# Optimization experiments

Measured on AMD Instinct MI355X. Metric: run time of the kernel, lower is better.

The kernel has to match this reference:

```python
import jax, jax.numpy as jnp
import numpy as np

DELTA = 0.5  # fuzziness factor (module default)

def setup_inputs() -> dict:
    key = jax.random.key(0)
    kq, kk, kv = jax.random.split(key, 3)
    B, L, H, E = 2, 2048, 16, 64
    queries = jax.random.normal(kq, (B, L, H, E), jnp.float32)
    keys_ = jax.random.normal(kk, (B, L, H, E), jnp.float32)
    values = jax.random.normal(kv, (B, L, H, E), jnp.float32)
    # TriangularCausalMask: True above the diagonal -> masked out
    attn_mask = jnp.triu(jnp.ones((L, L), dtype=bool), k=1)[None, None]  # [1,1,L,L]
    return {"queries": queries, "keys": keys_, "values": values, "attn_mask": attn_mask}

def reference(queries, keys, values, attn_mask):
    # queries: [B,L,H,E], keys/values: [B,S,H,E], attn_mask: [1,1,L,S] bool (True = masked)
    E = queries.shape[-1]
    scale = 1.0 / np.sqrt(E)
    scores = jnp.einsum('blhe,bshe->bhls', queries, keys)  # [B,H,L,S]
    # fuzzy modification; note sigmoid(-inf)=0 so masking before or after is equivalent,
    # we mask after for grad safety
    fuzzy = scores + DELTA * jax.nn.sigmoid(scores)
    fuzzy = jnp.where(attn_mask, -jnp.inf, fuzzy)
    A = jax.nn.softmax(scale * fuzzy, axis=-1)  # dropout p=0 (eval mode)
    V = jnp.einsum('bhls,bshd->blhd', A, values)  # [B,L,H,D]
    return V
```

## Files before the change

kernel.cpp:

```cpp
#include <hip/hip_runtime.h>
#include <math.h>


typedef __bf16 bf16x8 __attribute__((ext_vector_type(8)));
typedef __bf16 bf16x4 __attribute__((ext_vector_type(4)));
typedef float  f32x4  __attribute__((ext_vector_type(4)));

constexpr int Lc = 2048, Hc = 16, Ec = 64;
constexpr int QBLK = 64, KVB = 64;
constexpr int NQT  = Lc / QBLK;
constexpr int ROWS = Hc * Ec;
constexpr float LOG2E = 1.4426950408889634f;
constexpr float C1 = 0.125f * LOG2E;
constexpr float C3 = 0.5f * 0.125f * LOG2E;

__global__ __launch_bounds__(256)
void conv_kv(const float* __restrict__ Kp, const float* __restrict__ Vp,
             __bf16* __restrict__ Kbf, __bf16* __restrict__ Vbf) {
    const int bid = blockIdx.x;
    const int tid = threadIdx.x;
    if (bid < 1024) {
        const int task = bid * 256 + tid;
        const int row = task >> 2, q4 = task & 3;
        const int h = row & 15, bl = row >> 4;
        const int b = bl >> 11, l = bl & 2047;
        const float4* src = reinterpret_cast<const float4*>(Kp + (size_t)row * 64 + q4 * 16);
        __bf16* dst = Kbf + ((size_t)((b * 16 + h) * 2048 + l)) * 64 + q4 * 16;
        float4 x0 = src[0], x1 = src[1], x2 = src[2], x3 = src[3];
        bf16x8 o0, o1;
        o0[0]=(__bf16)x0.x; o0[1]=(__bf16)x0.y; o0[2]=(__bf16)x0.z; o0[3]=(__bf16)x0.w;
        o0[4]=(__bf16)x1.x; o0[5]=(__bf16)x1.y; o0[6]=(__bf16)x1.z; o0[7]=(__bf16)x1.w;
        o1[0]=(__bf16)x2.x; o1[1]=(__bf16)x2.y; o1[2]=(__bf16)x2.z; o1[3]=(__bf16)x2.w;
        o1[4]=(__bf16)x3.x; o1[5]=(__bf16)x3.y; o1[6]=(__bf16)x3.z; o1[7]=(__bf16)x3.w;
        reinterpret_cast<bf16x8*>(dst)[0] = o0;
        reinterpret_cast<bf16x8*>(dst)[1] = o1;
    } else {
        __shared__ __bf16 tl[64 * 72];
        const int vb = bid - 1024;
        const int bh = vb >> 5, lt = vb & 31;
        const int b = bh >> 4, h = bh & 15;
        {
            const int l = tid >> 2, dc = tid & 3;
            const float4* src = reinterpret_cast<const float4*>(
                Vp + ((size_t)((b * 2048 + lt * 64 + l) * 16 + h)) * 64 + dc * 16);
            float4 v0 = src[0], v1 = src[1], v2 = src[2], v3 = src[3];
            float e[16] = {v0.x,v0.y,v0.z,v0.w, v1.x,v1.y,v1.z,v1.w,
                           v2.x,v2.y,v2.z,v2.w, v3.x,v3.y,v3.z,v3.w};
            #pragma unroll
            for (int i = 0; i < 16; ++i) tl[(dc * 16 + i) * 72 + l] = (__bf16)e[i];
        }
        __syncthreads();
        {
            const int d = tid >> 2, lc = tid & 3;
            bf16x8 a = *reinterpret_cast<const bf16x8*>(&tl[d * 72 + lc * 16]);
            bf16x8 c = *reinterpret_cast<const bf16x8*>(&tl[d * 72 + lc * 16 + 8]);
            __bf16* dst = Vbf + ((size_t)bh * 64 + d) * 2048 + lt * 64 + lc * 16;
            reinterpret_cast<bf16x8*>(dst)[0] = a;
            reinterpret_cast<bf16x8*>(dst)[1] = c;
        }
    }
}

__global__ __launch_bounds__(256, 4)
void fuzzy_attn_mfma(const float* __restrict__ Qp, const __bf16* __restrict__ Kbf,
                     const __bf16* __restrict__ Vbf, float* __restrict__ Op) {
    __shared__ __bf16 kt[2][KVB * Ec];
    __shared__ __bf16 vt[2][KVB * Ec];
    __shared__ __bf16 pt[4][1024];

    const int id  = blockIdx.x;
    const int xcd = id & 7;
    const int r_  = id >> 3;
    const int s4  = r_ & 3;
    const int qt  = (NQT - 1) - (r_ >> 2);
    const int bh  = s4 * 8 + xcd;
    const int b = bh >> 4, h = bh & 15;

    const int tid  = threadIdx.x;
    const int lane = tid & 63;
    const int w    = tid >> 6;
    const int q16  = lane & 15;
    const int g    = lane >> 4;
    const int qhalf  = w & 1;
    const int kvhalf = w >> 1;

    const __bf16* Kh = Kbf + (size_t)bh * (Lc * Ec);
    const __bf16* Vh = Vbf + (size_t)bh * (Ec * Lc);
    const float*  Qb = Qp + (size_t)b * Lc * ROWS + h * Ec;
    float*        Ob = Op + (size_t)b * Lc * ROWS + h * Ec;

    const int qrow0 = qt * QBLK + qhalf * 32 + q16;
    const int qrow1 = qrow0 + 16;

    const int srow0 = w * 8 + (lane >> 3);
    const int srow1 = srow0 + 32;
    const int sch0  = (lane & 7) ^ ((srow0 & 7) ^ (srow0 >> 3));
    const int sch1  = (lane & 7) ^ ((srow1 & 7) ^ (srow1 >> 3));
    const __bf16* kgA = Kh + srow0 * 64   + sch0 * 8;
    const __bf16* kgB = Kh + srow1 * 64   + sch1 * 8;
    const __bf16* vgA = Vh + srow0 * 2048 + sch0 * 8;
    const __bf16* vgB = Vh + srow1 * 2048 + sch1 * 8;

    bf16x8 qb[2][2];
    #pragma unroll
    for (int qs = 0; qs < 2; ++qs) {
        #pragma unroll
        for (int ks = 0; ks < 2; ++ks) {
            const float* qp = Qb + (size_t)(qs ? qrow1 : qrow0) * ROWS + g * 8 + 32 * ks;
            float4 x0 = reinterpret_cast<const float4*>(qp)[0];
            float4 x1 = reinterpret_cast<const float4*>(qp)[1];
            bf16x8 tq;
            tq[0]=(__bf16)x0.x; tq[1]=(__bf16)x0.y; tq[2]=(__bf16)x0.z; tq[3]=(__bf16)x0.w;
            tq[4]=(__bf16)x1.x; tq[5]=(__bf16)x1.y; tq[6]=(__bf16)x1.z; tq[7]=(__bf16)x1.w;
            qb[qs][ks] = tq;
        }
    }

    const int nst = qt + 1;

    #define STAGE(bufi, st_)                                                          \
        do {                                                                          \
            const __bf16* kga = kgA + (size_t)(st_) * (KVB * Ec);                     \
            const __bf16* kgb = kgB + (size_t)(st_) * (KVB * Ec);                     \
            const __bf16* vga = vgA + (st_) * KVB;                                    \
            const __bf16* vgb = vgB + (st_) * KVB;                                    \
            __builtin_amdgcn_global_load_lds(                                         \
                (const __attribute__((address_space(1))) void*)kga,                   \
                (__attribute__((address_space(3))) void*)&kt[bufi][w * 512], 16, 0, 0); \
            __builtin_amdgcn_global_load_lds(                                         \
                (const __attribute__((address_space(1))) void*)kgb,                   \
                (__attribute__((address_space(3))) void*)&kt[bufi][2048 + w * 512], 16, 0, 0); \
            __builtin_amdgcn_global_load_lds(                                         \
                (const __attribute__((address_space(1))) void*)vga,                   \
                (__attribute__((address_space(3))) void*)&vt[bufi][w * 512], 16, 0, 0); \
            __builtin_amdgcn_global_load_lds(                                         \
                (const __attribute__((address_space(1))) void*)vgb,                   \
                (__attribute__((address_space(3))) void*)&vt[bufi][2048 + w * 512], 16, 0, 0); \
        } while (0)

    STAGE(0, 0);

    float la0 = 0.f, la1 = 0.f;
    float lb0 = 0.f, lb1 = 0.f;
    f32x4 oacc[2][4];
    #pragma unroll
    for (int qs = 0; qs < 2; ++qs) {
        #pragma unroll
        for (int ds = 0; ds < 4; ++ds) { f32x4 z = {0.f,0.f,0.f,0.f}; oacc[qs][ds] = z; }
    }

    char* pw = reinterpret_cast<char*>(pt[w]);
    const int pswz = q16 & 3;

    for (int st = 0; st < nst; ++st) {
        const int buf = st & 1;
        __syncthreads();

        if (st + 1 < nst) STAGE(buf ^ 1, st + 1);

        const char* kbase = reinterpret_cast<const char*>(kt[buf]);
        const char* vbase = reinterpret_cast<const char*>(vt[buf]);

        f32x4 sacc[2][2];
        #pragma unroll
        for (int kv = 0; kv < 2; ++kv) {
            #pragma unroll
            for (int qs = 0; qs < 2; ++qs) { f32x4 z = {0.f,0.f,0.f,0.f}; sacc[kv][qs] = z; }
        }
        __builtin_amdgcn_s_setprio(1);
        #pragma unroll
        for (int kv = 0; kv < 2; ++kv) {
            const int kvr  = kvhalf * 32 + kv * 16 + q16;
            const int kkey = ((kvr & 7) ^ (kvr >> 3)) << 4;
            #pragma unroll
            for (int ks = 0; ks < 2; ++ks) {
                bf16x8 ka = *reinterpret_cast<const bf16x8*>(
                    kbase + kvr * 128 + (((g + 4 * ks) << 4) ^ kkey));
                sacc[kv][0] = __builtin_amdgcn_mfma_f32_16x16x32_bf16(ka, qb[0][ks], sacc[kv][0], 0, 0, 0);
                sacc[kv][1] = __builtin_amdgcn_mfma_f32_16x16x32_bf16(ka, qb[1][ks], sacc[kv][1], 0, 0, 0);
            }
        }
        __builtin_amdgcn_s_setprio(0);

        const bool diagm = (st == qt) && (kvhalf >= qhalf);
        #pragma unroll
        for (int kv = 0; kv < 2; ++kv) {
            #pragma unroll
            for (int qs = 0; qs < 2; ++qs) {
                const int qrow_s = qs ? qrow1 : qrow0;
                float p4[4];
                #pragma unroll
                for (int r = 0; r < 4; ++r) {
                    const float s  = sacc[kv][qs][r];
                    const float sg = __builtin_amdgcn_fmed3f(fmaf(s, 0.1875f, 0.5f), 0.f, 1.f);
                    float u = fmaf(sg, C3, s * C1);
                    if (diagm) {
                        const int kvg = st * KVB + kvhalf * 32 + kv * 16 + 4 * g + r;
                        if (kvg > qrow_s) u = -INFINITY;
                    }
                    p4[r] = __builtin_amdgcn_exp2f(u);
                }
                if (qs == 0) { la0 += p4[0] + p4[1]; la1 += p4[2] + p4[3]; }
                else         { lb0 += p4[0] + p4[1]; lb1 += p4[2] + p4[3]; }
                bf16x4 pk;
                pk[0]=(__bf16)p4[0]; pk[1]=(__bf16)p4[1]; pk[2]=(__bf16)p4[2]; pk[3]=(__bf16)p4[3];
                *reinterpret_cast<bf16x4*>(
                    pw + (qs * 16 + q16) * 64 +
                    (((2 * kv + (g >> 1)) ^ pswz) << 4) + (g & 1) * 8) = pk;
            }
        }

        bf16x8 pa0 = *reinterpret_cast<const bf16x8*>(
            pw + (0 * 16 + q16) * 64 + ((g ^ pswz) << 4));
        bf16x8 pa1 = *reinterpret_cast<const bf16x8*>(
            pw + (1 * 16 + q16) * 64 + ((g ^ pswz) << 4));
        __builtin_amdgcn_s_setprio(1);
        #pragma unroll
        for (int ds = 0; ds < 4; ++ds) {
            const int vrow = ds * 16 + q16;
            const int vkey = ((vrow & 7) ^ (vrow >> 3)) << 4;
            bf16x8 vb = *reinterpret_cast<const bf16x8*>(
                vbase + vrow * 128 + (((kvhalf * 4 + g) << 4) ^ vkey));
            oacc[0][ds] = __builtin_amdgcn_mfma_f32_16x16x32_bf16(pa0, vb, oacc[0][ds], 0, 0, 0);
            oacc[1][ds] = __builtin_amdgcn_mfma_f32_16x16x32_bf16(pa1, vb, oacc[1][ds], 0, 0, 0);
        }
        __builtin_amdgcn_s_setprio(0);
    }
    #undef STAGE

    float lr0 = la0 + la1;
    float lr1 = lb0 + lb1;
    lr0 += __shfl_xor(lr0, 16); lr0 += __shfl_xor(lr0, 32);
    lr1 += __shfl_xor(lr1, 16); lr1 += __shfl_xor(lr1, 32);

    __syncthreads();
    float* sc = reinterpret_cast<float*>(kt);
    float* ls = reinterpret_cast<float*>(vt);

    if (kvhalf == 1) {
        #pragma unroll
        for (int qs = 0; qs < 2; ++qs) {
            #pragma unroll
            for (int ds = 0; ds < 4; ++ds) {
                #pragma unroll
                for (int r = 0; r < 4; ++r) {
                    sc[qhalf * 2048 + (qs * 16 + g * 4 + r) * 64 + ds * 16 + q16] =
                        oacc[qs][ds][r];
                }
            }
        }
    }
    if (lane < 16) {
        ls[(qhalf * 2 + kvhalf) * 32 + q16]      = lr0;
        ls[(qhalf * 2 + kvhalf) * 32 + 16 + q16] = lr1;
    }
    __syncthreads();

    if (kvhalf == 0) {
        const float inv0 = 1.f / (lr0 + ls[(qhalf * 2 + 1) * 32 + q16]);
        const float inv1 = 1.f / (lr1 + ls[(qhalf * 2 + 1) * 32 + 16 + q16]);
        float i40[4], i41[4];
        #pragma unroll
        for (int r = 0; r < 4; ++r) { i40[r] = __shfl(inv0, g * 4 + r);
                                      i41[r] = __shfl(inv1, g * 4 + r); }
        #pragma unroll
        for (int qs = 0; qs < 2; ++qs) {
            #pragma unroll
            for (int ds = 0; ds < 4; ++ds) {
                #pragma unroll
                for (int r = 0; r < 4; ++r) {
                    const int qlocal = qs * 16 + g * 4 + r;
                    const int row = qt * QBLK + qhalf * 32 + qlocal;
                    const float o = oacc[qs][ds][r] +
                        sc[qhalf * 2048 + qlocal * 64 + ds * 16 + q16];
                    const float sv = qs ? i41[r] : i40[r];
                    Ob[(size_t)row * ROWS + ds * 16 + q16] = o * sv;
                }
            }
        }
    }
}

extern "C" void kernel_launch(void* const* d_in, const int* in_sizes, int n_in,
                              void* d_out, int out_size, void* d_ws, size_t ws_size,
                              hipStream_t stream) {
    (void)in_sizes; (void)n_in; (void)out_size; (void)ws_size;
    const float* Q = (const float*)d_in[0];
    const float* K = (const float*)d_in[1];
    const float* V = (const float*)d_in[2];
    float* O = (float*)d_out;

    __bf16* Kbf = (__bf16*)d_ws;
    __bf16* Vbf = (__bf16*)((char*)d_ws + (size_t)32 * 2048 * 64 * 2);

    conv_kv<<<dim3(2048), dim3(256), 0, stream>>>(K, V, Kbf, Vbf);
    fuzzy_attn_mfma<<<dim3(1024), dim3(256), 0, stream>>>(Q, Kbf, Vbf, O);
}
```

Measured before the change: 56.33 us.

## Single-buffer K/V in LDS with staggered loads to raise occupancy

Replaces the double-buffered K and V LDS tiles with single buffers in one 24 KB shared array. V for the current step is loaded during the QK/softmax phase, and K for the next step is loaded during the PV phase. Launch bounds go from 4 to 6 blocks per CU. This cuts LDS use so more blocks fit per CU, at the cost of an extra barrier per iteration and less latency hiding per block. V loads now have to complete within the softmax window.

```diff
diff --git a/kernel.cpp b/kernel.cpp
--- a/kernel.cpp
+++ b/kernel.cpp
@@ -61,12 +61,12 @@
     }
 }
 
-__global__ __launch_bounds__(256, 4)
+__global__ __launch_bounds__(256, 6)
 void fuzzy_attn_mfma(const float* __restrict__ Qp, const __bf16* __restrict__ Kbf,
                      const __bf16* __restrict__ Vbf, float* __restrict__ Op) {
-    __shared__ __bf16 kt[2][KVB * Ec];
-    __shared__ __bf16 vt[2][KVB * Ec];
-    __shared__ __bf16 pt[4][1024];
+    __shared__ char smem[24576];
+    __bf16* kt0 = reinterpret_cast<__bf16*>(smem);
+    __bf16* vt0 = reinterpret_cast<__bf16*>(smem + 8192);
 
     const int id  = blockIdx.x;
     const int xcd = id & 7;
@@ -118,27 +118,31 @@
 
     const int nst = qt + 1;
 
-    #define STAGE(bufi, st_)                                                          \
+    #define STAGE_K(st_)                                                              \
         do {                                                                          \
             const __bf16* kga = kgA + (size_t)(st_) * (KVB * Ec);                     \
             const __bf16* kgb = kgB + (size_t)(st_) * (KVB * Ec);                     \
+            __builtin_amdgcn_global_load_lds(                                         \
+                (const __attribute__((address_space(1))) void*)kga,                   \
+                (__attribute__((address_space(3))) void*)&kt0[w * 512], 16, 0, 0);    \
+            __builtin_amdgcn_global_load_lds(                                         \
+                (const __attribute__((address_space(1))) void*)kgb,                   \
+                (__attribute__((address_space(3))) void*)&kt0[2048 + w * 512], 16, 0, 0); \
+        } while (0)
+    #define STAGE_V(st_)                                                              \
+        do {                                                                          \
             const __bf16* vga = vgA + (st_) * KVB;                                    \
             const __bf16* vgb = vgB + (st_) * KVB;                                    \
             __builtin_amdgcn_global_load_lds(                                         \
-                (const __attribute__((address_space(1))) void*)kga,                   \
-                (__attribute__((address_space(3))) void*)&kt[bufi][w * 512], 16, 0, 0); \
-            __builtin_amdgcn_global_load_lds(                                         \
-                (const __attribute__((address_space(1))) void*)kgb,                   \
-                (__attribute__((address_space(3))) void*)&kt[bufi][2048 + w * 512], 16, 0, 0); \
-            __builtin_amdgcn_global_load_lds(                                         \
                 (const __attribute__((address_space(1))) void*)vga,                   \
-                (__attribute__((address_space(3))) void*)&vt[bufi][w * 512], 16, 0, 0); \
+                (__attribute__((address_space(3))) void*)&vt0[w * 512], 16, 0, 0);    \
             __builtin_amdgcn_global_load_lds(                                         \
                 (const __attribute__((address_space(1))) void*)vgb,                   \
-                (__attribute__((address_space(3))) void*)&vt[bufi][2048 + w * 512], 16, 0, 0); \
+                (__attribute__((address_space(3))) void*)&vt0[2048 + w * 512], 16, 0, 0); \
         } while (0)
 
-    STAGE(0, 0);
+    STAGE_K(0);
+    __syncthreads();
 
     float la0 = 0.f, la1 = 0.f;
     float lb0 = 0.f, lb1 = 0.f;
@@ -149,17 +153,14 @@
         for (int ds = 0; ds < 4; ++ds) { f32x4 z = {0.f,0.f,0.f,0.f}; oacc[qs][ds] = z; }
     }
 
-    char* pw = reinterpret_cast<char*>(pt[w]);
+    char* pw = smem + 16384 + w * 2048;
     const int pswz = q16 & 3;
 
+    const char* kbase = reinterpret_cast<const char*>(kt0);
+    const char* vbase = reinterpret_cast<const char*>(vt0);
+
     for (int st = 0; st < nst; ++st) {
-        const int buf = st & 1;
-        __syncthreads();
-
-        if (st + 1 < nst) STAGE(buf ^ 1, st + 1);
-
-        const char* kbase = reinterpret_cast<const char*>(kt[buf]);
-        const char* vbase = reinterpret_cast<const char*>(vt[buf]);
+        STAGE_V(st);
 
         f32x4 sacc[2][2];
         #pragma unroll
@@ -210,6 +211,10 @@
             }
         }
 
+        __syncthreads();
+
+        if (st + 1 < nst) STAGE_K(st + 1);
+
         bf16x8 pa0 = *reinterpret_cast<const bf16x8*>(
             pw + (0 * 16 + q16) * 64 + ((g ^ pswz) << 4));
         bf16x8 pa1 = *reinterpret_cast<const bf16x8*>(
@@ -225,17 +230,19 @@
             oacc[1][ds] = __builtin_amdgcn_mfma_f32_16x16x32_bf16(pa1, vb, oacc[1][ds], 0, 0, 0);
         }
         __builtin_amdgcn_s_setprio(0);
-    }
-    #undef STAGE
+
+        __syncthreads();
+    }
+    #undef STAGE_K
+    #undef STAGE_V
 
     float lr0 = la0 + la1;
     float lr1 = lb0 + lb1;
     lr0 += __shfl_xor(lr0, 16); lr0 += __shfl_xor(lr0, 32);
     lr1 += __shfl_xor(lr1, 16); lr1 += __shfl_xor(lr1, 32);
 
-    __syncthreads();
-    float* sc = reinterpret_cast<float*>(kt);
-    float* ls = reinterpret_cast<float*>(vt);
+    float* sc = reinterpret_cast<float*>(smem);
+    float* ls = reinterpret_cast<float*>(smem + 16384);
 
     if (kvhalf == 1) {
         #pragma unroll
```

After: 99.52 us. 76.7% more time.
